# Kernel tuning notes

Measured on AMD Instinct MI355X. Metric: run time of the kernel, lower is better.

## Reference

```python
import jax, jax.numpy as jnp
import numpy as np

GAMMA = 0.99


def setup_inputs() -> dict:
    key = jax.random.key(0)
    ks = jax.random.split(key, 6)
    T, D, H = 65536, 1024, 1024
    s1 = 1.0 / np.sqrt(D)
    s2 = 1.0 / np.sqrt(H)
    return {
        "rewards": jax.random.normal(ks[0], (T,), jnp.float32),
        "obs": jax.random.normal(ks[1], (T, D), jnp.float32),
        "W1": jax.random.normal(ks[2], (D, H), jnp.float32) * s1,
        "b1": jnp.zeros((H,), jnp.float32),
        "W2": jax.random.normal(ks[3], (H, H), jnp.float32) * s2,
        "b2": jnp.zeros((H,), jnp.float32),
        "W3": jax.random.normal(ks[4], (H, 1), jnp.float32) * s2,
        "b3": jnp.zeros((1,), jnp.float32),
    }


def _discounted_returns(rewards):
    # G[i] = r[i] + gamma * G[i+1], computed as a reverse scan
    def step(g, r):
        g = r + GAMMA * g
        return g, g
    _, G = jax.lax.scan(step, jnp.zeros((), rewards.dtype), rewards, reverse=True)
    return G


def reference(rewards, obs, W1, b1, W2, b2, W3, b3):
    G = _discounted_returns(rewards)              # [T]
    h = jax.nn.relu(obs @ W1 + b1)                # [T, H]
    h = jax.nn.relu(h @ W2 + b2)                  # [T, H]
    V = (h @ W3 + b3).reshape(-1)                 # [T]
    return G - V
```

## Files before the change

kernel.cpp:

```cpp
#include <hip/hip_runtime.h>

typedef __bf16 bf16x8 __attribute__((ext_vector_type(8)));
typedef __bf16 bf16x4 __attribute__((ext_vector_type(4)));
typedef float  f32x4  __attribute__((ext_vector_type(4)));

#define GAMMA 0.99f

__device__ __forceinline__ void gload_lds16(const void* g, void* l) {
  __builtin_amdgcn_global_load_lds(
      (const __attribute__((address_space(1))) void*)g,
      (__attribute__((address_space(3))) void*)l, 16, 0, 0);
}

#define VMCNT0() asm volatile("s_waitcnt vmcnt(0)" ::: "memory")
#define BAR() __builtin_amdgcn_s_barrier()
#define MFMA(d, a, b) d = __builtin_amdgcn_mfma_f32_16x16x32_bf16(a, b, d, 0, 0, 0)

__global__ __launch_bounds__(1024) void mega_prep(
    const float* __restrict__ rw, float* __restrict__ G,
    const float* __restrict__ obs, __bf16* __restrict__ obsb,
    const float* __restrict__ W1, const float* __restrict__ W2,
    __bf16* __restrict__ BT1, __bf16* __restrict__ BT2, int nObs) {
  __shared__ float smem[4224];
  const int blk = blockIdx.x;
  const int t = threadIdx.x;
  if (blk == 0) {
    float* sv = smem;
    const float4* rp = (const float4*)(rw + t * 64);
    float4 lv[16];
#pragma unroll
    for (int i = 0; i < 16; ++i) lv[i] = rp[i];
    float loc[64];
#pragma unroll
    for (int i = 0; i < 16; ++i) {
      loc[4 * i + 0] = lv[i].x; loc[4 * i + 1] = lv[i].y;
      loc[4 * i + 2] = lv[i].z; loc[4 * i + 3] = lv[i].w;
    }
    float g = 0.f;
#pragma unroll
    for (int j = 63; j >= 0; --j) { g = loc[j] + GAMMA * g; loc[j] = g; }
    sv[t] = g;
    float W = GAMMA;
#pragma unroll
    for (int i = 0; i < 6; ++i) W *= W;
    float v = g;
    for (int s = 1; s < 1024; s <<= 1) {
      __syncthreads();
      float o = (t + s < 1024) ? sv[t + s] : 0.f;
      __syncthreads();
      v += W * o;
      sv[t] = v;
      W *= W;
    }
    __syncthreads();
    const float nxt = (t < 1023) ? sv[t + 1] : 0.f;
    float pw = GAMMA;
#pragma unroll
    for (int j = 63; j >= 0; --j) {
      G[t * 64 + j] = loc[j] + pw * nxt;
      pw *= GAMMA;
    }
  } else if (blk <= nObs) {
    const size_t base = (size_t)(blk - 1) * 32768 + (size_t)t * 8;
#pragma unroll
    for (int it = 0; it < 4; ++it) {
      const size_t e = base + (size_t)it * 8192;
      float4 u0 = *(const float4*)(obs + e);
      float4 u1 = *(const float4*)(obs + e + 4);
      bf16x8 o = {(__bf16)u0.x, (__bf16)u0.y, (__bf16)u0.z, (__bf16)u0.w,
                  (__bf16)u1.x, (__bf16)u1.y, (__bf16)u1.z, (__bf16)u1.w};
      *(bf16x8*)(obsb + e) = o;
    }
  } else {
    const int sub = t >> 8, tt = t & 255;
    const int wi = (blk - nObs - 1) * 4 + sub;
    const float* W = (wi >= 1024) ? W2 : W1;
    __bf16* O = (wi >= 1024) ? BT2 : BT1;
    const int tile = wi & 1023;
    const int ti = tile >> 5, tj = tile & 31;
    float* s = smem + sub * 1056;
    const int rr = tt >> 3, c4 = (tt & 7) * 4;
    float4 v = *(const float4*)(W + (size_t)(ti * 32 + rr) * 1024 + tj * 32 + c4);
    s[rr * 33 + c4 + 0] = v.x; s[rr * 33 + c4 + 1] = v.y;
    s[rr * 33 + c4 + 2] = v.z; s[rr * 33 + c4 + 3] = v.w;
    __syncthreads();
    bf16x4 o = {(__bf16)s[(c4 + 0) * 33 + rr], (__bf16)s[(c4 + 1) * 33 + rr],
                (__bf16)s[(c4 + 2) * 33 + rr], (__bf16)s[(c4 + 3) * 33 + rr]};
    *(bf16x4*)(O + (size_t)(tj * 32 + rr) * 1024 + ti * 32 + c4) = o;
  }
}

#define GEMM_KLOOP(APTR, BPTR)                                                 \
  extern __shared__ char lds[];                                                \
  const int t = threadIdx.x, lane = t & 63, w = t >> 6;                        \
  const int wsr = w >> 2, wsc = w & 3, g = lane >> 4, l15 = lane & 15;         \
  const int bid = blockIdx.x;                                                  \
  const int mb = (bid & 7) * 32 + ((bid >> 3) >> 2);                           \
  const int nb = (bid >> 3) & 3;                                               \
  const size_t stg_off =                                                       \
      (size_t)(t >> 2) * 2048 + (size_t)(((t & 3) ^ ((t >> 3) & 3)) * 16);     \
  const char* Ag = (const char*)(APTR) + (size_t)mb * 524288 + stg_off;        \
  const char* Bg = (const char*)(BPTR) + (size_t)nb * 524288 + stg_off;        \
  const int csw = (g ^ ((l15 >> 1) & 3)) << 4;                                 \
  const int arb = (wsr * 64 + l15) * 64 + csw;                                 \
  const int brb = (wsc * 32 + l15) * 64 + csw + 16384;                         \
  f32x4 acc[2][4][2][2];                                                       \
  const f32x4 zero = {0.f, 0.f, 0.f, 0.f};                                     \
  _Pragma("unroll") for (int a_ = 0; a_ < 2; ++a_)                             \
  _Pragma("unroll") for (int b_ = 0; b_ < 4; ++b_)                             \
  _Pragma("unroll") for (int c_ = 0; c_ < 2; ++c_)                             \
  _Pragma("unroll") for (int d_ = 0; d_ < 2; ++d_)                             \
    acc[a_][b_][c_][d_] = zero;                                                \
  auto STA = [&](int buf, int kt) {                                            \
    const char* s = Ag + kt * 64;                                              \
    char* d = lds + buf * 32768 + t * 16;                                      \
    gload_lds16(s, d);                                                         \
    gload_lds16(s + 262144, d + 8192);                                         \
  };                                                                           \
  auto STB = [&](int buf, int kt) {                                            \
    const char* s = Bg + kt * 64;                                              \
    char* d = lds + buf * 32768 + 16384 + t * 16;                              \
    gload_lds16(s, d);                                                         \
    gload_lds16(s + 262144, d + 8192);                                         \
  };                                                                           \
  STA(0, 0);                                                                   \
  STB(0, 0);                                                                   \
  VMCNT0();                                                                    \
  BAR();                                                                       \
  int cur = 0;                                                                 \
  for (int kt = 0; kt < 32; ++kt) {                                            \
    const int nx = cur ^ 1;                                                    \
    const char* ab = lds + cur * 32768;                                        \
    if (kt < 31) STA(nx, kt + 1);                                              \
    bf16x8 bfr[2][2];                                                          \
    _Pragma("unroll") for (int nh = 0; nh < 2; ++nh)                           \
    _Pragma("unroll") for (int j = 0; j < 2; ++j)                              \
      bfr[nh][j] = *(const bf16x8*)(ab + brb + (nh * 128 + j * 16) * 64);      \
    if (kt < 31) STB(nx, kt + 1);                                              \
    bf16x8 afr[4];                                                             \
    _Pragma("unroll") for (int i = 0; i < 4; ++i)                              \
      afr[i] = *(const bf16x8*)(ab + arb + (i * 16) * 64);                     \
    __builtin_amdgcn_s_setprio(1);                                             \
    _Pragma("unroll") for (int i = 0; i < 4; ++i)                              \
    _Pragma("unroll") for (int nh = 0; nh < 2; ++nh)                           \
    _Pragma("unroll") for (int j = 0; j < 2; ++j)                              \
      MFMA(acc[0][i][nh][j], afr[i], bfr[nh][j]);                              \
    __builtin_amdgcn_s_setprio(0);                                             \
    _Pragma("unroll") for (int i = 0; i < 4; ++i)                              \
      afr[i] = *(const bf16x8*)(ab + arb + ((128 + i * 16) * 64));             \
    __builtin_amdgcn_s_setprio(1);                                             \
    _Pragma("unroll") for (int i = 0; i < 4; ++i)                              \
    _Pragma("unroll") for (int nh = 0; nh < 2; ++nh)                           \
    _Pragma("unroll") for (int j = 0; j < 2; ++j)                              \
      MFMA(acc[1][i][nh][j], afr[i], bfr[nh][j]);                              \
    __builtin_amdgcn_s_setprio(0);                                             \
    if (kt < 31) VMCNT0();                                                     \
    BAR();                                                                     \
    cur = nx;                                                                  \
  }

__global__ __launch_bounds__(512, 2) void gemm1(
    const __bf16* __restrict__ obsb, const __bf16* __restrict__ BT1,
    const float* __restrict__ b1, __bf16* __restrict__ h1) {
  GEMM_KLOOP(obsb, BT1)
  float b1v[2][2];
#pragma unroll
  for (int nh = 0; nh < 2; ++nh)
#pragma unroll
    for (int j = 0; j < 2; ++j)
      b1v[nh][j] = b1[nb * 256 + nh * 128 + wsc * 32 + j * 16 + l15];
  const int rr = t >> 2, qt = t & 3, grr = (rr >> 2) & 3;
#pragma unroll
  for (int mh = 0; mh < 2; ++mh) {
    __syncthreads();
#pragma unroll
    for (int i = 0; i < 4; ++i)
#pragma unroll
      for (int nh = 0; nh < 2; ++nh)
#pragma unroll
        for (int j = 0; j < 2; ++j)
#pragma unroll
          for (int reg = 0; reg < 4; ++reg) {
            float v = acc[mh][i][nh][j][reg] + b1v[nh][j];
            v = v > 0.f ? v : 0.f;
            const int Rl = wsr * 64 + i * 16 + g * 4 + reg;
            const int Cb = nh * 256 + wsc * 64 + j * 32 + l15 * 2;
            *(__bf16*)(lds + Rl * 512 + (Cb ^ (g << 5))) = (__bf16)v;
          }
    __syncthreads();
    char* dp = (char*)h1 + (size_t)(mb * 256 + mh * 128 + rr) * 2048 +
               nb * 512 + qt * 128;
    const char* sp = lds + rr * 512;
#pragma unroll
    for (int q = 0; q < 8; ++q) {
      const int qe = (q + t) & 7;
      *(f32x4*)(dp + qe * 16) =
          *(const f32x4*)(sp + ((qt * 128 + qe * 16) ^ (grr << 5)));
    }
  }
}

__global__ __launch_bounds__(512, 2) void gemm2(
    const __bf16* __restrict__ h1, const __bf16* __restrict__ BT2,
    const float* __restrict__ b2, const float* __restrict__ W3,
    float* __restrict__ V4) {
  GEMM_KLOOP(h1, BT2)
  float b2v[2][2], w3v[2][2];
#pragma unroll
  for (int nh = 0; nh < 2; ++nh)
#pragma unroll
    for (int j = 0; j < 2; ++j) {
      const int C = nb * 256 + nh * 128 + wsc * 32 + j * 16 + l15;
      b2v[nh][j] = b2[C];
      w3v[nh][j] = W3[C];
    }
  float p[2][4][4];
#pragma unroll
  for (int mh = 0; mh < 2; ++mh)
#pragma unroll
    for (int i = 0; i < 4; ++i)
#pragma unroll
      for (int reg = 0; reg < 4; ++reg) {
        float s = 0.f;
#pragma unroll
        for (int nh = 0; nh < 2; ++nh)
#pragma unroll
          for (int j = 0; j < 2; ++j) {
            float v = acc[mh][i][nh][j][reg] + b2v[nh][j];
            v = v > 0.f ? v : 0.f;
            s += v * w3v[nh][j];
          }
        p[mh][i][reg] = s;
      }
#pragma unroll
  for (int d = 1; d < 16; d <<= 1)
#pragma unroll
    for (int mh = 0; mh < 2; ++mh)
#pragma unroll
      for (int i = 0; i < 4; ++i)
#pragma unroll
        for (int reg = 0; reg < 4; ++reg)
          p[mh][i][reg] += __shfl_xor(p[mh][i][reg], d, 64);
  float* vp = (float*)lds;
  if (l15 == 0) {
#pragma unroll
    for (int mh = 0; mh < 2; ++mh)
#pragma unroll
      for (int i = 0; i < 4; ++i)
#pragma unroll
        for (int reg = 0; reg < 4; ++reg)
          vp[wsc * 256 + mh * 128 + wsr * 64 + i * 16 + g * 4 + reg] =
              p[mh][i][reg];
  }
  __syncthreads();
  if (t < 256) {
    float s = vp[t] + vp[256 + t] + vp[512 + t] + vp[768 + t];
    V4[(size_t)nb * 65536 + mb * 256 + t] = s;
  }
}

__global__ __launch_bounds__(256) void final_kernel(const float* __restrict__ G,
                                                    const float* __restrict__ V4,
                                                    const float* __restrict__ b3,
                                                    float* __restrict__ out) {
  int i = blockIdx.x * 256 + threadIdx.x;
  out[i] = G[i] - (V4[i] + V4[65536 + i] + V4[131072 + i] + V4[196608 + i] + b3[0]);
}

extern "C" void kernel_launch(void* const* d_in, const int* in_sizes, int n_in,
                              void* d_out, int out_size, void* d_ws, size_t ws_size,
                              hipStream_t stream) {
  const float* rewards = (const float*)d_in[0];
  const float* obs = (const float*)d_in[1];
  const float* W1 = (const float*)d_in[2];
  const float* b1 = (const float*)d_in[3];
  const float* W2 = (const float*)d_in[4];
  const float* b2 = (const float*)d_in[5];
  const float* W3 = (const float*)d_in[6];
  const float* b3 = (const float*)d_in[7];
  float* out = (float*)d_out;

  char* ws = (char*)d_ws;
  __bf16* BT1 = (__bf16*)(ws);
  __bf16* BT2 = (__bf16*)(ws + (2u << 20));
  float* V4 = (float*)(ws + (4u << 20));
  float* G = (float*)(ws + (5u << 20));
  __bf16* obsb = (__bf16*)(ws + (8u << 20));
  __bf16* h1 = (__bf16*)(ws + (136u << 20));

  hipFuncSetAttribute((const void*)gemm1,
                      hipFuncAttributeMaxDynamicSharedMemorySize, 65536);
  hipFuncSetAttribute((const void*)gemm2,
                      hipFuncAttributeMaxDynamicSharedMemorySize, 65536);

  mega_prep<<<1 + 2048 + 512, 1024, 0, stream>>>(rewards, G, obs, obsb, W1, W2,
                                                 BT1, BT2, 2048);
  gemm1<<<1024, 512, 65536, stream>>>(obsb, BT1, b1, h1);
  gemm2<<<1024, 512, 65536, stream>>>(h1, BT2, b2, W3, V4);
  final_kernel<<<256, 256, 0, stream>>>(G, V4, b3, out);
}
```

Before: 378.2 us.

## Swap MFMA operands to transpose accumulator layout and simplify epilogues

Swaps the A/B operands of the MFMA so that each lane holds four consecutive output columns for one row instead of four rows for one column. The gemm1 epilogue then writes bf16x4 directly to global memory, dropping the LDS staging, its two barriers and the swizzled copy-out. The gemm2 epilogue reduces the four columns in-lane and needs two cross-lane shuffles instead of four rounds over sixteen values. The trade-off is narrower 8-byte global stores that are less coalesced than the previous 16-byte row-contiguous stores.

```diff
diff --git a/kernel.cpp b/kernel.cpp
--- a/kernel.cpp
+++ b/kernel.cpp
@@ -144,7 +144,7 @@
     _Pragma("unroll") for (int i = 0; i < 4; ++i)                              \
     _Pragma("unroll") for (int nh = 0; nh < 2; ++nh)                           \
     _Pragma("unroll") for (int j = 0; j < 2; ++j)                              \
-      MFMA(acc[0][i][nh][j], afr[i], bfr[nh][j]);                              \
+      MFMA(acc[0][i][nh][j], bfr[nh][j], afr[i]);                              \
     __builtin_amdgcn_s_setprio(0);                                             \
     _Pragma("unroll") for (int i = 0; i < 4; ++i)                              \
       afr[i] = *(const bf16x8*)(ab + arb + ((128 + i * 16) * 64));             \
@@ -152,7 +152,7 @@
     _Pragma("unroll") for (int i = 0; i < 4; ++i)                              \
     _Pragma("unroll") for (int nh = 0; nh < 2; ++nh)                           \
     _Pragma("unroll") for (int j = 0; j < 2; ++j)                              \
-      MFMA(acc[1][i][nh][j], afr[i], bfr[nh][j]);                              \
+      MFMA(acc[1][i][nh][j], bfr[nh][j], afr[i]);                              \
     __builtin_amdgcn_s_setprio(0);                                             \
     if (kt < 31) VMCNT0();                                                     \
     BAR();                                                                     \
@@ -163,41 +163,34 @@
     const __bf16* __restrict__ obsb, const __bf16* __restrict__ BT1,
     const float* __restrict__ b1, __bf16* __restrict__ h1) {
   GEMM_KLOOP(obsb, BT1)
-  float b1v[2][2];
+  f32x4 b1q[2][2];
 #pragma unroll
   for (int nh = 0; nh < 2; ++nh)
 #pragma unroll
     for (int j = 0; j < 2; ++j)
-      b1v[nh][j] = b1[nb * 256 + nh * 128 + wsc * 32 + j * 16 + l15];
-  const int rr = t >> 2, qt = t & 3, grr = (rr >> 2) & 3;
-#pragma unroll
-  for (int mh = 0; mh < 2; ++mh) {
-    __syncthreads();
-#pragma unroll
-    for (int i = 0; i < 4; ++i)
+      b1q[nh][j] =
+          *(const f32x4*)(b1 + nb * 256 + nh * 128 + wsc * 32 + j * 16 + g * 4);
+#pragma unroll
+  for (int mh = 0; mh < 2; ++mh)
+#pragma unroll
+    for (int i = 0; i < 4; ++i) {
+      const size_t mrow = (size_t)(mb * 256 + mh * 128 + wsr * 64 + i * 16 + l15);
 #pragma unroll
       for (int nh = 0; nh < 2; ++nh)
 #pragma unroll
-        for (int j = 0; j < 2; ++j)
-#pragma unroll
-          for (int reg = 0; reg < 4; ++reg) {
-            float v = acc[mh][i][nh][j][reg] + b1v[nh][j];
-            v = v > 0.f ? v : 0.f;
-            const int Rl = wsr * 64 + i * 16 + g * 4 + reg;
-            const int Cb = nh * 256 + wsc * 64 + j * 32 + l15 * 2;
-            *(__bf16*)(lds + Rl * 512 + (Cb ^ (g << 5))) = (__bf16)v;
-          }
-    __syncthreads();
-    char* dp = (char*)h1 + (size_t)(mb * 256 + mh * 128 + rr) * 2048 +
-               nb * 512 + qt * 128;
-    const char* sp = lds + rr * 512;
-#pragma unroll
-    for (int q = 0; q < 8; ++q) {
-      const int qe = (q + t) & 7;
-      *(f32x4*)(dp + qe * 16) =
-          *(const f32x4*)(sp + ((qt * 128 + qe * 16) ^ (grr << 5)));
-    }
-  }
+        for (int j = 0; j < 2; ++j) {
+          f32x4 v = acc[mh][i][nh][j];
+          v.x += b1q[nh][j].x; v.y += b1q[nh][j].y;
+          v.z += b1q[nh][j].z; v.w += b1q[nh][j].w;
+          v.x = v.x > 0.f ? v.x : 0.f;
+          v.y = v.y > 0.f ? v.y : 0.f;
+          v.z = v.z > 0.f ? v.z : 0.f;
+          v.w = v.w > 0.f ? v.w : 0.f;
+          bf16x4 o = {(__bf16)v.x, (__bf16)v.y, (__bf16)v.z, (__bf16)v.w};
+          *(bf16x4*)(h1 + mrow * 1024 + nb * 256 + nh * 128 + wsc * 32 +
+                     j * 16 + g * 4) = o;
+        }
+    }
 }
 
 __global__ __launch_bounds__(512, 2) void gemm2(
@@ -205,52 +198,51 @@
     const float* __restrict__ b2, const float* __restrict__ W3,
     float* __restrict__ V4) {
   GEMM_KLOOP(h1, BT2)
-  float b2v[2][2], w3v[2][2];
+  f32x4 b2q[2][2], w3q[2][2];
 #pragma unroll
   for (int nh = 0; nh < 2; ++nh)
 #pragma unroll
     for (int j = 0; j < 2; ++j) {
-      const int C = nb * 256 + nh * 128 + wsc * 32 + j * 16 + l15;
-      b2v[nh][j] = b2[C];
-      w3v[nh][j] = W3[C];
-    }
-  float p[2][4][4];
+      const int C = nb * 256 + nh * 128 + wsc * 32 + j * 16 + g * 4;
+      b2q[nh][j] = *(const f32x4*)(b2 + C);
+      w3q[nh][j] = *(const f32x4*)(W3 + C);
+    }
+  float p[2][4];
 #pragma unroll
   for (int mh = 0; mh < 2; ++mh)
 #pragma unroll
-    for (int i = 0; i < 4; ++i)
-#pragma unroll
-      for (int reg = 0; reg < 4; ++reg) {
-        float s = 0.f;
-#pragma unroll
-        for (int nh = 0; nh < 2; ++nh)
-#pragma unroll
-          for (int j = 0; j < 2; ++j) {
-            float v = acc[mh][i][nh][j][reg] + b2v[nh][j];
-            v = v > 0.f ? v : 0.f;
-            s += v * w3v[nh][j];
-          }
-        p[mh][i][reg] = s;
-      }
-#pragma unroll
-  for (int d = 1; d < 16; d <<= 1)
+    for (int i = 0; i < 4; ++i) {
+      float s = 0.f;
+#pragma unroll
+      for (int nh = 0; nh < 2; ++nh)
+#pragma unroll
+        for (int j = 0; j < 2; ++j) {
+          f32x4 v = acc[mh][i][nh][j];
+          v.x += b2q[nh][j].x; v.y += b2q[nh][j].y;
+          v.z += b2q[nh][j].z; v.w += b2q[nh][j].w;
+          v.x = v.x > 0.f ? v.x : 0.f;
+          v.y = v.y > 0.f ? v.y : 0.f;
+          v.z = v.z > 0.f ? v.z : 0.f;
+          v.w = v.w > 0.f ? v.w : 0.f;
+          s += v.x * w3q[nh][j].x + v.y * w3q[nh][j].y +
+               v.z * w3q[nh][j].z + v.w * w3q[nh][j].w;
+        }
+      p[mh][i] = s;
+    }
+#pragma unroll
+  for (int mh = 0; mh < 2; ++mh)
+#pragma unroll
+    for (int i = 0; i < 4; ++i) {
+      p[mh][i] += __shfl_xor(p[mh][i], 16, 64);
+      p[mh][i] += __shfl_xor(p[mh][i], 32, 64);
+    }
+  float* vp = (float*)lds;
+  if (g == 0) {
 #pragma unroll
     for (int mh = 0; mh < 2; ++mh)
 #pragma unroll
       for (int i = 0; i < 4; ++i)
-#pragma unroll
-        for (int reg = 0; reg < 4; ++reg)
-          p[mh][i][reg] += __shfl_xor(p[mh][i][reg], d, 64);
-  float* vp = (float*)lds;
-  if (l15 == 0) {
-#pragma unroll
-    for (int mh = 0; mh < 2; ++mh)
-#pragma unroll
-      for (int i = 0; i < 4; ++i)
-#pragma unroll
-        for (int reg = 0; reg < 4; ++reg)
-          vp[wsc * 256 + mh * 128 + wsr * 64 + i * 16 + g * 4 + reg] =
-              p[mh][i][reg];
+        vp[wsc * 256 + mh * 128 + wsr * 64 + i * 16 + l15] = p[mh][i];
   }
   __syncthreads();
   if (t < 256) {
```

Measured after the change: 357.7 us. 1.06x faster.
